# Performance work log

Hardware: AMD Instinct MI355X
Metric: run time of the kernel (lower is better)

Reference implementation:

```python
import jax, jax.numpy as jnp
import numpy as np

T, B, IN, H, L = 512, 64, 512, 1024, 2
EPS = 1e-5


def setup_inputs() -> dict:
    key = jax.random.key(0)
    ks = jax.random.split(key, 10)
    s_in = 1.0 / np.sqrt(H)  # torch init: U(-sqrt(1/hidden), sqrt(1/hidden))
    u = lambda k, shape: jax.random.uniform(k, shape, jnp.float32, -s_in, s_in)
    return {
        "input": jax.random.normal(ks[0], (T, B, IN), jnp.float32),
        "hidden": jax.random.normal(ks[1], (L, B, H), jnp.float32) * 0.1,
        "W_ih0": u(ks[2], (H, IN)),
        "W_hh0": u(ks[3], (H, H)),
        "b_ih0": u(ks[4], (H,)),
        "b_hh0": u(ks[5], (H,)),
        "ln_w0": jnp.ones((H,), jnp.float32),
        "ln_b0": jnp.zeros((H,), jnp.float32),
        "W_ih1": u(ks[6], (H, H)),
        "W_hh1": u(ks[7], (H, H)),
        "b_ih1": u(ks[8], (H,)),
        "b_hh1": u(ks[9], (H,)),
        "ln_w1": jnp.ones((H,), jnp.float32),
        "ln_b1": jnp.zeros((H,), jnp.float32),
    }


def _cell(x, h, W_ih, W_hh, b, ln_w, ln_b):
    # pre = [x, h] @ [W_ih, W_hh]^T + (b_ih + b_hh)   -> [B, H]
    pre = x @ W_ih.T + h @ W_hh.T + b
    mu = jnp.mean(pre, axis=-1, keepdims=True)
    var = jnp.var(pre, axis=-1, keepdims=True)
    y = (pre - mu) * jax.lax.rsqrt(var + EPS) * ln_w + ln_b  # LayerNorm
    return jnp.tanh(y)


def reference(input, hidden, W_ih0, W_hh0, b_ih0, b_hh0, ln_w0, ln_b0,
              W_ih1, W_hh1, b_ih1, b_hh1, ln_w1, ln_b1):
    b0 = b_ih0 + b_hh0
    b1 = b_ih1 + b_hh1

    def step(h, x_t):  # h: [L, B, H], x_t: [B, IN]
        h0 = _cell(x_t, h[0], W_ih0, W_hh0, b0, ln_w0, ln_b0)
        h1 = _cell(h0, h[1], W_ih1, W_hh1, b1, ln_w1, ln_b1)
        return jnp.stack([h0, h1]), h1

    h_fin, out = jax.lax.scan(step, hidden, input)
    return (out, h_fin)  # out: [T, B, H], h_fin: [L, B, H]
```

## Files before the change

kernel.cpp:

```cpp
#include <hip/hip_runtime.h>
#include <stdint.h>

#define T_ 512
#define B_ 64
#define IN_ 512
#define H_ 1024
#define RB 16
#define LNEPS 1e-5f
#define ZSCALE 2.885390081777927f
#define FL(t, rg) (((t) * 4 + (rg)) * 32)

typedef __attribute__((ext_vector_type(8))) _Float16 h16x8;
typedef __attribute__((ext_vector_type(2))) _Float16 h16x2;
typedef __attribute__((ext_vector_type(4))) float f32x4;
typedef __attribute__((ext_vector_type(4))) float float4v;
typedef __attribute__((ext_vector_type(4))) int int4v;
typedef unsigned short ushort_t;

__device__ __forceinline__ h16x8 ldw8h(const float* p) {
  float4v a = *(const float4v*)p;
  float4v b = *(const float4v*)(p + 4);
  h16x8 o;
  o[0] = (_Float16)a[0]; o[1] = (_Float16)a[1]; o[2] = (_Float16)a[2]; o[3] = (_Float16)a[3];
  o[4] = (_Float16)b[0]; o[5] = (_Float16)b[1]; o[6] = (_Float16)b[2]; o[7] = (_Float16)b[3];
  return o;
}
#define PIN8(x) asm volatile("" : "+v"(x))

__device__ __forceinline__ void sth_sys(ushort_t* p, float v) {
  _Float16 h = (_Float16)v;
  int s = (int)__builtin_bit_cast(short, h);
  asm volatile("global_store_short %0, %1, off sc0 sc1" :: "v"(p), "v"(s) : "memory");
}
__device__ __forceinline__ void relfence() { asm volatile("s_waitcnt vmcnt(0)" ::: "memory"); }
__device__ __forceinline__ void stamp16(ushort_t* p, int v) {
  asm volatile("global_store_short %0, %1, off sc0 sc1" :: "v"(p), "v"(v) : "memory");
}
__device__ __forceinline__ void poll32h(const ushort_t* p, int target) {
  int n = 0;
  while (true) {
    int4v a, b, c, d;
    asm volatile(
        "global_load_dwordx4 %0, %4, off sc0 sc1\n\t"
        "global_load_dwordx4 %1, %4, off offset:16 sc0 sc1\n\t"
        "global_load_dwordx4 %2, %4, off offset:32 sc0 sc1\n\t"
        "global_load_dwordx4 %3, %4, off offset:48 sc0 sc1\n\t"
        "s_waitcnt vmcnt(0)"
        : "=&v"(a), "=&v"(b), "=&v"(c), "=&v"(d) : "v"(p) : "memory");
    int mn = 0xFFFF;
#pragma unroll
    for (int i = 0; i < 4; ++i) {
      unsigned u0 = (unsigned)a[i], u1 = (unsigned)b[i], u2 = (unsigned)c[i], u3 = (unsigned)d[i];
      mn = min(mn, (int)(u0 & 0xFFFFu)); mn = min(mn, (int)(u0 >> 16));
      mn = min(mn, (int)(u1 & 0xFFFFu)); mn = min(mn, (int)(u1 >> 16));
      mn = min(mn, (int)(u2 & 0xFFFFu)); mn = min(mn, (int)(u2 >> 16));
      mn = min(mn, (int)(u3 & 0xFFFFu)); mn = min(mn, (int)(u3 >> 16));
    }
    if (mn >= target) return;
    if (n < 4) __builtin_amdgcn_s_sleep(1);
    else __builtin_amdgcn_s_sleep(4);
    if (++n > 2000000) return;
  }
}

__device__ __forceinline__ int chix(int r, int c) {
  int ch = c >> 3;
  int low = ((ch >> 3) ^ ch ^ r) & 3;
  return r * 1032 + ((((ch >> 2) << 2) | low) << 3) + (c & 7);
}

__device__ __forceinline__ void stageHf(const float* src, ushort_t* dA, int tid) {
  int r = tid >> 5, k = tid & 31, c0 = k * 32;
  const float* p = src + (size_t)r * H_ + c0;
#pragma unroll
  for (int q = 0; q < 4; ++q) {
    float4v a = *(const float4v*)(p + q * 8);
    float4v b = *(const float4v*)(p + q * 8 + 4);
    h16x8 h;
    h[0] = (_Float16)a[0]; h[1] = (_Float16)a[1]; h[2] = (_Float16)a[2]; h[3] = (_Float16)a[3];
    h[4] = (_Float16)b[0]; h[5] = (_Float16)b[1]; h[6] = (_Float16)b[2]; h[7] = (_Float16)b[3];
    *(h16x8*)&dA[chix(r, c0 + q * 8)] = h;
  }
}
__device__ __forceinline__ void stageXh(const float* src, ushort_t* dA, int tid) {
  int r = tid >> 5, k = tid & 31, c0 = k * 16;
  const float* p = src + (size_t)r * IN_ + c0;
#pragma unroll
  for (int q = 0; q < 2; ++q) {
    float4v a = *(const float4v*)(p + q * 8);
    float4v b = *(const float4v*)(p + q * 8 + 4);
    h16x8 h;
    h[0] = (_Float16)a[0]; h[1] = (_Float16)a[1]; h[2] = (_Float16)a[2]; h[3] = (_Float16)a[3];
    h[4] = (_Float16)b[0]; h[5] = (_Float16)b[1]; h[6] = (_Float16)b[2]; h[7] = (_Float16)b[3];
    *(h16x8*)&dA[chix(r, c0 + q * 8)] = h;
  }
}
__device__ __forceinline__ void ldraw4(const ushort_t* src, h16x8 (&raw)[4], int tid) {
  int r = tid >> 5, k = tid & 31, c0 = k * 32;
  const ushort_t* p = src + (size_t)r * H_ + c0;
#pragma unroll
  for (int q = 0; q < 4; ++q) raw[q] = *(const h16x8*)(p + q * 8);
}
__device__ __forceinline__ void procLTh(const h16x8 (&raw)[4], ushort_t* dA,
                                        const _Float16* lnw, const _Float16* lnbz, int tid,
                                        int cg, bool wr, float* gA, float* gB) {
  int r = tid >> 5, k = tid & 31, c0 = k * 32;
  const h16x2 one2 = {(_Float16)1.f, (_Float16)1.f};
  float s = 0.f, ss = 0.f;
#pragma unroll
  for (int q = 0; q < 4; ++q) {
#pragma unroll
    for (int pp = 0; pp < 4; ++pp) {
      h16x2 xp;
      xp[0] = raw[q][2 * pp]; xp[1] = raw[q][2 * pp + 1];
      s = __builtin_amdgcn_fdot2(xp, one2, s, false);
      ss = __builtin_amdgcn_fdot2(xp, xp, ss, false);
    }
  }
#pragma unroll
  for (int m = 1; m <= 16; m <<= 1) { s += __shfl_xor(s, m, 64); ss += __shfl_xor(ss, m, 64); }
  float mu = s * (1.f / H_);
  float var = ss * (1.f / H_) - mu * mu;
  float zrs = rsqrtf(var + LNEPS) * ZSCALE;
  _Float16 muh = (_Float16)mu, zrsh = (_Float16)zrs;
  h16x2 mu2 = {muh, muh}, zrs2 = {zrsh, zrsh};
#pragma unroll
  for (int q = 0; q < 4; ++q) {
    h16x8 wv = *(const h16x8*)&lnw[q * 256 + k * 8];
    h16x8 bzv = *(const h16x8*)&lnbz[q * 256 + k * 8];
    h16x8 hout;
    float hf[8];
#pragma unroll
    for (int pp = 0; pp < 4; ++pp) {
      h16x2 xp, wp, bp;
      xp[0] = raw[q][2 * pp]; xp[1] = raw[q][2 * pp + 1];
      wp[0] = wv[2 * pp];     wp[1] = wv[2 * pp + 1];
      bp[0] = bzv[2 * pp];    bp[1] = bzv[2 * pp + 1];
      h16x2 z2 = (xp - mu2) * zrs2 * wp + bp;
#pragma unroll
      for (int e = 0; e < 2; ++e) {
        float z = (float)z2[e];
        z = fminf(15.8f, fmaxf(-15.8f, z));
        float ex = __builtin_amdgcn_exp2f(z);
        float rr = __builtin_amdgcn_rcpf(ex + 1.f);
        float hv = __builtin_fmaf(-2.f, rr, 1.f);
        hout[2 * pp + e] = (_Float16)hv;
        hf[2 * pp + e] = hv;
      }
    }
    *(h16x8*)&dA[chix(r, c0 + q * 8)] = hout;
    if (wr && k == cg) {
      float* pa = gA + (size_t)r * H_ + c0 + q * 8;
      *(float4v*)pa = (float4v){hf[0], hf[1], hf[2], hf[3]};
      *(float4v*)(pa + 4) = (float4v){hf[4], hf[5], hf[6], hf[7]};
      if (gB) {
        float* pb = gB + (size_t)r * H_ + c0 + q * 8;
        *(float4v*)pb = (float4v){hf[0], hf[1], hf[2], hf[3]};
        *(float4v*)(pb + 4) = (float4v){hf[4], hf[5], hf[6], hf[7]};
      }
    }
  }
}
__device__ __forceinline__ void stageLTh(const ushort_t* src, ushort_t* dA,
                                         const _Float16* lnw, const _Float16* lnbz, int tid,
                                         int cg, bool wr, float* gA, float* gB) {
  h16x8 raw[4];
  ldraw4(src, raw, tid);
  procLTh(raw, dA, lnw, lnbz, tid, cg, wr, gA, gB);
}

#define MFMA(a, b, c) __builtin_amdgcn_mfma_f32_16x16x32_f16(a, b, c, 0, 0, 0)
#define AF(buf, idx) (*(const h16x8*)&buf[chix(lane & 15, (idx) + kb8)])

__global__ __launch_bounds__(512, 1) void rnn_persist(
    const float* __restrict__ input, const float* __restrict__ hidden,
    const float* __restrict__ W_ih0, const float* __restrict__ W_hh0,
    const float* __restrict__ b_ih0, const float* __restrict__ b_hh0,
    const float* __restrict__ ln_w0, const float* __restrict__ ln_b0,
    const float* __restrict__ W_ih1, const float* __restrict__ W_hh1,
    const float* __restrict__ b_ih1, const float* __restrict__ b_hh1,
    const float* __restrict__ ln_w1, const float* __restrict__ ln_b1,
    float* gout, ushort_t* pre0, ushort_t* pre1,
    ushort_t* flag0a, ushort_t* flag0b, ushort_t* flag1a) {
  __shared__ ushort_t sA[16 * 1032];
  __shared__ ushort_t sA1[16 * 1032];
  __shared__ _Float16 slnw0h[1024], slnbz0h[1024];
  __shared__ _Float16 slnw1h[1024], slnbz1h[1024];
  __shared__ float sacc[3][2][16][16];

  const int tid = threadIdx.x;
  const int lane = tid & 63;
  const int w = tid >> 6;
  const int colt = w & 1, kh = w >> 1;
  const int blk = blockIdx.x;
  const int layer = (blk >> 2) & 1;
  const int rg = blk & 3;
  const int cg = blk >> 3;
  const int rowbase = rg * RB;
  const int cgl = cg * 32 + colt * 16 + (lane & 15);
  const int kb8 = (lane >> 4) * 8;
  const int l15 = lane & 15;

  for (int i = tid; i < H_; i += 512) {
    int kk = i >> 5, rem = i & 31, q = rem >> 3, j = rem & 7;
    int pi = q * 256 + kk * 8 + j;
    slnw0h[pi] = (_Float16)ln_w0[i];
    slnbz0h[pi] = (_Float16)(ZSCALE * ln_b0[i]);
    slnw1h[pi] = (_Float16)ln_w1[i];
    slnbz1h[pi] = (_Float16)(ZSCALE * ln_b1[i]);
  }

  float bias = 0.f;

  if (layer == 0) {
    h16x8 WX[4], WH[8];
#pragma unroll
    for (int s = 0; s < 4; ++s) {
      WX[s] = ldw8h(W_ih0 + (size_t)cgl * IN_ + kh * 128 + s * 32 + kb8);
      PIN8(WX[s]);
    }
#pragma unroll
    for (int s = 0; s < 8; ++s) {
      WH[s] = ldw8h(W_hh0 + (size_t)cgl * H_ + kh * 256 + s * 32 + kb8);
      PIN8(WH[s]);
    }
    if (kh == 0) bias = b_ih0[cgl] + b_hh0[cgl];
    __syncthreads();

    for (int t = 0; t < T_; ++t) {
      stageXh(input + ((size_t)t * B_ + rowbase) * IN_, sA, tid);
      __syncthreads();
      f32x4 acc = (kh == 0) ? (f32x4){bias, bias, bias, bias} : (f32x4){0.f, 0.f, 0.f, 0.f};
#pragma unroll
      for (int s = 0; s < 4; ++s) acc = MFMA(AF(sA, kh * 128 + s * 32), WX[s], acc);
      if (tid == 0 && t > 0) poll32h(&flag0a[FL(t - 1, rg)], t);
      __syncthreads();
      if (t == 0) stageHf(hidden + (size_t)rowbase * H_, sA, tid);
      else stageLTh(pre0 + ((size_t)(t - 1) * B_ + rowbase) * H_, sA,
                    slnw0h, slnbz0h, tid, cg, false, nullptr, nullptr);
      __syncthreads();
#pragma unroll
      for (int s = 0; s < 8; ++s) acc = MFMA(AF(sA, kh * 256 + s * 32), WH[s], acc);
      if (kh > 0) {
#pragma unroll
        for (int j = 0; j < 4; ++j) sacc[kh - 1][colt][(lane >> 4) * 4 + j][l15] = acc[j];
      }
      __syncthreads();
      if (kh == 0) {
        ushort_t* dst = pre0 + ((size_t)t * B_ + rowbase) * H_;
#pragma unroll
        for (int j = 0; j < 4; ++j) {
          int row = (lane >> 4) * 4 + j;
          float v = acc[j] + sacc[0][colt][row][l15] + sacc[1][colt][row][l15] +
                    sacc[2][colt][row][l15];
          sth_sys(&dst[(size_t)row * H_ + cgl], v);
        }
        relfence();
      }
      __syncthreads();
      if (tid == 0) {
        stamp16(&flag0a[FL(t, rg) + cg], t + 1);
        stamp16(&flag0b[FL(t, rg) + cg], t + 1);
      }
    }
    if (tid == 0) poll32h(&flag0a[FL(T_ - 1, rg)], T_);
    __syncthreads();
    stageLTh(pre0 + ((size_t)(T_ - 1) * B_ + rowbase) * H_, sA, slnw0h, slnbz0h, tid, cg, true,
             gout + (size_t)T_ * B_ * H_ + (size_t)rowbase * H_, nullptr);
  } else {
    h16x8 WB[8], WA[8];
#pragma unroll
    for (int s = 0; s < 8; ++s) {
      WB[s] = ldw8h(W_ih1 + (size_t)cgl * H_ + kh * 256 + s * 32 + kb8);
      PIN8(WB[s]);
    }
#pragma unroll
    for (int s = 0; s < 8; ++s) {
      WA[s] = ldw8h(W_hh1 + (size_t)cgl * H_ + kh * 256 + s * 32 + kb8);
      PIN8(WA[s]);
    }
    if (kh == 0) bias = b_ih1[cgl] + b_hh1[cgl];
    __syncthreads();

    for (int t = 0; t < T_; ++t) {
      if (tid == 0) poll32h(&flag0b[FL(t, rg)], t + 1);
      __syncthreads();
      stageLTh(pre0 + ((size_t)t * B_ + rowbase) * H_, sA,
               slnw0h, slnbz0h, tid, cg, false, nullptr, nullptr);
      if (tid == 64 && t > 0) poll32h(&flag1a[FL(t - 1, rg)], t);
      __syncthreads();
      f32x4 acc = (kh == 0) ? (f32x4){bias, bias, bias, bias} : (f32x4){0.f, 0.f, 0.f, 0.f};
      if (t == 0) {
#pragma unroll
        for (int s = 0; s < 8; ++s) acc = MFMA(AF(sA, kh * 256 + s * 32), WB[s], acc);
        stageHf(hidden + (size_t)B_ * H_ + (size_t)rowbase * H_, sA1, tid);
      } else {
        h16x8 raw1[4];
        ldraw4(pre1 + ((size_t)(t - 1) * B_ + rowbase) * H_, raw1, tid);
#pragma unroll
        for (int s = 0; s < 8; ++s) acc = MFMA(AF(sA, kh * 256 + s * 32), WB[s], acc);
        procLTh(raw1, sA1, slnw1h, slnbz1h, tid, cg, true,
                gout + ((size_t)(t - 1) * B_ + rowbase) * H_, nullptr);
      }
      __syncthreads();
#pragma unroll
      for (int s = 0; s < 8; ++s) acc = MFMA(AF(sA1, kh * 256 + s * 32), WA[s], acc);
      if (kh > 0) {
#pragma unroll
        for (int j = 0; j < 4; ++j) sacc[kh - 1][colt][(lane >> 4) * 4 + j][l15] = acc[j];
      }
      __syncthreads();
      if (kh == 0) {
        ushort_t* dst = pre1 + ((size_t)t * B_ + rowbase) * H_;
#pragma unroll
        for (int j = 0; j < 4; ++j) {
          int row = (lane >> 4) * 4 + j;
          float v = acc[j] + sacc[0][colt][row][l15] + sacc[1][colt][row][l15] +
                    sacc[2][colt][row][l15];
          sth_sys(&dst[(size_t)row * H_ + cgl], v);
        }
        relfence();
      }
      __syncthreads();
      if (tid == 0) stamp16(&flag1a[FL(t, rg) + cg], t + 1);
    }
    if (tid == 0) poll32h(&flag1a[FL(T_ - 1, rg)], T_);
    __syncthreads();
    stageLTh(pre1 + ((size_t)(T_ - 1) * B_ + rowbase) * H_, sA, slnw1h, slnbz1h, tid, cg, true,
             gout + ((size_t)(T_ - 1) * B_ + rowbase) * H_,
             gout + (size_t)T_ * B_ * H_ + (size_t)B_ * H_ + (size_t)rowbase * H_);
  }
}

extern "C" void kernel_launch(void* const* d_in, const int* in_sizes, int n_in,
                              void* d_out, int out_size, void* d_ws, size_t ws_size,
                              hipStream_t stream) {
  const float* input = (const float*)d_in[0];
  const float* hidden = (const float*)d_in[1];
  const float* W_ih0 = (const float*)d_in[2];
  const float* W_hh0 = (const float*)d_in[3];
  const float* b_ih0 = (const float*)d_in[4];
  const float* b_hh0 = (const float*)d_in[5];
  const float* ln_w0 = (const float*)d_in[6];
  const float* ln_b0 = (const float*)d_in[7];
  const float* W_ih1 = (const float*)d_in[8];
  const float* W_hh1 = (const float*)d_in[9];
  const float* b_ih1 = (const float*)d_in[10];
  const float* b_hh1 = (const float*)d_in[11];
  const float* ln_w1 = (const float*)d_in[12];
  const float* ln_b1 = (const float*)d_in[13];
  float* gout = (float*)d_out;

  const size_t slabT = (size_t)T_ * B_ * H_ * 2;
  char* ws = (char*)d_ws;
  ushort_t* pre0 = (ushort_t*)ws;
  ushort_t* pre1 = (ushort_t*)(ws + slabT);
  char* ctrl = ws + 2 * slabT;
  ushort_t* flag0a = (ushort_t*)ctrl;
  ushort_t* flag0b = (ushort_t*)(ctrl + 0x20000);
  ushort_t* flag1a = (ushort_t*)(ctrl + 0x40000);

  (void)hipMemsetAsync(ctrl, 0, 0x60000, stream);
  hipLaunchKernelGGL(rnn_persist, dim3(256), dim3(512), 0, stream,
                     input, hidden, W_ih0, W_hh0, b_ih0, b_hh0, ln_w0, ln_b0,
                     W_ih1, W_hh1, b_ih1, b_hh1, ln_w1, ln_b1,
                     gout, pre0, pre1, flag0a, flag0b, flag1a);
}
```

Measured before the change: 3.008 ms.

## Use per-wave flag stamps and overlap layer-0 input GEMM with hidden-state load

Flag slots per timestep and row group double to 64, so each kh==0 wave stamps its own flag right after its release fence, not after a block-wide barrier. Pollers now check 64 half-word flags. In layer 0 the input tile goes to a separate LDS buffer, and the poll moves before the first barrier. The previous-step pre-activation is loaded into registers while the input MFMAs run, then normalized into LDS, which drops one barrier per step. The cost is twice the flag traffic per poll and a larger flag memset.

```diff
diff --git a/kernel.cpp b/kernel.cpp
--- a/kernel.cpp
+++ b/kernel.cpp
@@ -8,7 +8,7 @@
 #define RB 16
 #define LNEPS 1e-5f
 #define ZSCALE 2.885390081777927f
-#define FL(t, rg) (((t) * 4 + (rg)) * 32)
+#define FL(t, rg) (((t) * 4 + (rg)) * 64)
 
 typedef __attribute__((ext_vector_type(8))) _Float16 h16x8;
 typedef __attribute__((ext_vector_type(2))) _Float16 h16x2;
@@ -36,25 +36,36 @@
 __device__ __forceinline__ void stamp16(ushort_t* p, int v) {
   asm volatile("global_store_short %0, %1, off sc0 sc1" :: "v"(p), "v"(v) : "memory");
 }
-__device__ __forceinline__ void poll32h(const ushort_t* p, int target) {
+__device__ __forceinline__ void poll64h(const ushort_t* p, int target) {
   int n = 0;
   while (true) {
-    int4v a, b, c, d;
+    int4v a, b, c, d, e, f, g, h;
     asm volatile(
-        "global_load_dwordx4 %0, %4, off sc0 sc1\n\t"
-        "global_load_dwordx4 %1, %4, off offset:16 sc0 sc1\n\t"
-        "global_load_dwordx4 %2, %4, off offset:32 sc0 sc1\n\t"
-        "global_load_dwordx4 %3, %4, off offset:48 sc0 sc1\n\t"
+        "global_load_dwordx4 %0, %8, off sc0 sc1\n\t"
+        "global_load_dwordx4 %1, %8, off offset:16 sc0 sc1\n\t"
+        "global_load_dwordx4 %2, %8, off offset:32 sc0 sc1\n\t"
+        "global_load_dwordx4 %3, %8, off offset:48 sc0 sc1\n\t"
+        "global_load_dwordx4 %4, %8, off offset:64 sc0 sc1\n\t"
+        "global_load_dwordx4 %5, %8, off offset:80 sc0 sc1\n\t"
+        "global_load_dwordx4 %6, %8, off offset:96 sc0 sc1\n\t"
+        "global_load_dwordx4 %7, %8, off offset:112 sc0 sc1\n\t"
         "s_waitcnt vmcnt(0)"
-        : "=&v"(a), "=&v"(b), "=&v"(c), "=&v"(d) : "v"(p) : "memory");
+        : "=&v"(a), "=&v"(b), "=&v"(c), "=&v"(d),
+          "=&v"(e), "=&v"(f), "=&v"(g), "=&v"(h)
+        : "v"(p) : "memory");
     int mn = 0xFFFF;
 #pragma unroll
     for (int i = 0; i < 4; ++i) {
       unsigned u0 = (unsigned)a[i], u1 = (unsigned)b[i], u2 = (unsigned)c[i], u3 = (unsigned)d[i];
+      unsigned u4 = (unsigned)e[i], u5 = (unsigned)f[i], u6 = (unsigned)g[i], u7 = (unsigned)h[i];
       mn = min(mn, (int)(u0 & 0xFFFFu)); mn = min(mn, (int)(u0 >> 16));
       mn = min(mn, (int)(u1 & 0xFFFFu)); mn = min(mn, (int)(u1 >> 16));
       mn = min(mn, (int)(u2 & 0xFFFFu)); mn = min(mn, (int)(u2 >> 16));
       mn = min(mn, (int)(u3 & 0xFFFFu)); mn = min(mn, (int)(u3 >> 16));
+      mn = min(mn, (int)(u4 & 0xFFFFu)); mn = min(mn, (int)(u4 >> 16));
+      mn = min(mn, (int)(u5 & 0xFFFFu)); mn = min(mn, (int)(u5 >> 16));
+      mn = min(mn, (int)(u6 & 0xFFFFu)); mn = min(mn, (int)(u6 >> 16));
+      mn = min(mn, (int)(u7 & 0xFFFFu)); mn = min(mn, (int)(u7 >> 16));
     }
     if (mn >= target) return;
     if (n < 4) __builtin_amdgcn_s_sleep(1);
@@ -228,16 +239,21 @@
     __syncthreads();
 
     for (int t = 0; t < T_; ++t) {
-      stageXh(input + ((size_t)t * B_ + rowbase) * IN_, sA, tid);
+      stageXh(input + ((size_t)t * B_ + rowbase) * IN_, sA1, tid);
+      if (tid == 0 && t > 0) poll64h(&flag0a[FL(t - 1, rg)], t);
       __syncthreads();
       f32x4 acc = (kh == 0) ? (f32x4){bias, bias, bias, bias} : (f32x4){0.f, 0.f, 0.f, 0.f};
-#pragma unroll
-      for (int s = 0; s < 4; ++s) acc = MFMA(AF(sA, kh * 128 + s * 32), WX[s], acc);
-      if (tid == 0 && t > 0) poll32h(&flag0a[FL(t - 1, rg)], t);
-      __syncthreads();
-      if (t == 0) stageHf(hidden + (size_t)rowbase * H_, sA, tid);
-      else stageLTh(pre0 + ((size_t)(t - 1) * B_ + rowbase) * H_, sA,
-                    slnw0h, slnbz0h, tid, cg, false, nullptr, nullptr);
+      if (t == 0) {
+#pragma unroll
+        for (int s = 0; s < 4; ++s) acc = MFMA(AF(sA1, kh * 128 + s * 32), WX[s], acc);
+        stageHf(hidden + (size_t)rowbase * H_, sA, tid);
+      } else {
+        h16x8 raw[4];
+        ldraw4(pre0 + ((size_t)(t - 1) * B_ + rowbase) * H_, raw, tid);
+#pragma unroll
+        for (int s = 0; s < 4; ++s) acc = MFMA(AF(sA1, kh * 128 + s * 32), WX[s], acc);
+        procLTh(raw, sA, slnw0h, slnbz0h, tid, cg, false, nullptr, nullptr);
+      }
       __syncthreads();
 #pragma unroll
       for (int s = 0; s < 8; ++s) acc = MFMA(AF(sA, kh * 256 + s * 32), WH[s], acc);
@@ -256,14 +272,13 @@
           sth_sys(&dst[(size_t)row * H_ + cgl], v);
         }
         relfence();
-      }
-      __syncthreads();
-      if (tid == 0) {
-        stamp16(&flag0a[FL(t, rg) + cg], t + 1);
-        stamp16(&flag0b[FL(t, rg) + cg], t + 1);
-      }
-    }
-    if (tid == 0) poll32h(&flag0a[FL(T_ - 1, rg)], T_);
+        if (lane == 0) {
+          stamp16(&flag0a[FL(t, rg) + colt * 32 + cg], t + 1);
+          stamp16(&flag0b[FL(t, rg) + colt * 32 + cg], t + 1);
+        }
+      }
+    }
+    if (tid == 0) poll64h(&flag0a[FL(T_ - 1, rg)], T_);
     __syncthreads();
     stageLTh(pre0 + ((size_t)(T_ - 1) * B_ + rowbase) * H_, sA, slnw0h, slnbz0h, tid, cg, true,
              gout + (size_t)T_ * B_ * H_ + (size_t)rowbase * H_, nullptr);
@@ -283,11 +298,11 @@
     __syncthreads();
 
     for (int t = 0; t < T_; ++t) {
-      if (tid == 0) poll32h(&flag0b[FL(t, rg)], t + 1);
+      if (tid == 0) poll64h(&flag0b[FL(t, rg)], t + 1);
       __syncthreads();
       stageLTh(pre0 + ((size_t)t * B_ + rowbase) * H_, sA,
                slnw0h, slnbz0h, tid, cg, false, nullptr, nullptr);
-      if (tid == 64 && t > 0) poll32h(&flag1a[FL(t - 1, rg)], t);
+      if (tid == 64 && t > 0) poll64h(&flag1a[FL(t - 1, rg)], t);
       __syncthreads();
       f32x4 acc = (kh == 0) ? (f32x4){bias, bias, bias, bias} : (f32x4){0.f, 0.f, 0.f, 0.f};
       if (t == 0) {
@@ -320,11 +335,10 @@
           sth_sys(&dst[(size_t)row * H_ + cgl], v);
         }
         relfence();
-      }
-      __syncthreads();
-      if (tid == 0) stamp16(&flag1a[FL(t, rg) + cg], t + 1);
-    }
-    if (tid == 0) poll32h(&flag1a[FL(T_ - 1, rg)], T_);
+        if (lane == 0) stamp16(&flag1a[FL(t, rg) + colt * 32 + cg], t + 1);
+      }
+    }
+    if (tid == 0) poll64h(&flag1a[FL(T_ - 1, rg)], T_);
     __syncthreads();
     stageLTh(pre1 + ((size_t)(T_ - 1) * B_ + rowbase) * H_, sA, slnw1h, slnbz1h, tid, cg, true,
              gout + ((size_t)(T_ - 1) * B_ + rowbase) * H_,
@@ -357,10 +371,10 @@
   ushort_t* pre1 = (ushort_t*)(ws + slabT);
   char* ctrl = ws + 2 * slabT;
   ushort_t* flag0a = (ushort_t*)ctrl;
-  ushort_t* flag0b = (ushort_t*)(ctrl + 0x20000);
-  ushort_t* flag1a = (ushort_t*)(ctrl + 0x40000);
-
-  (void)hipMemsetAsync(ctrl, 0, 0x60000, stream);
+  ushort_t* flag0b = (ushort_t*)(ctrl + 0x40000);
+  ushort_t* flag1a = (ushort_t*)(ctrl + 0x80000);
+
+  (void)hipMemsetAsync(ctrl, 0, 0xC0000, stream);
   hipLaunchKernelGGL(rnn_persist, dim3(256), dim3(512), 0, stream,
                      input, hidden, W_ih0, W_hh0, b_ih0, b_hh0, ln_w0, ln_b0,
                      W_ih1, W_hh1, b_ih1, b_hh1, ln_w1, ln_b1,
```

Result: slower. 3.113 ms (+3.5%).
